# Kernel optimization log

Hardware: AMD Instinct MI355X
Metric: run time of the kernel (lower is better)

Reference implementation:

```python
import jax, jax.numpy as jnp
import numpy as np

S, WD, TD, CE, CH = 512, 300, 100, 20, 20   # seq len, word dim, tag dim, char emb dim, char lstm hidden
H = 512                                      # main LSTM hidden (per direction)
VOC, TVOC, CVOC, LAB, MAXW = 50000, 50, 100, 50, 16


def lstm_scan(x, W_ih, W_hh, b):
    """Unidirectional LSTM over x:[T,D] -> [T,hid]. PyTorch gate order i,f,g,o."""
    hid = W_hh.shape[1]
    def step(carry, xt):
        h, c = carry
        z = xt @ W_ih.T + h @ W_hh.T + b
        i, f, g, o = jnp.split(z, 4)
        c = jax.nn.sigmoid(f) * c + jax.nn.sigmoid(i) * jnp.tanh(g)
        h = jax.nn.sigmoid(o) * jnp.tanh(c)
        return (h, c), h
    h0 = jnp.zeros((hid,), x.dtype)
    _, hs = jax.lax.scan(step, (h0, h0), x)
    return hs


def setup_inputs() -> dict:
    key = jax.random.key(0)
    ks = jax.random.split(key, 40)
    n = lambda i, shape: jax.random.normal(ks[i], shape, jnp.float32) * 0.05
    return {
        "sentence": jax.random.randint(ks[0], (S,), 0, VOC),
        "tags": jax.random.randint(ks[1], (S,), 0, TVOC),
        "chars": jax.random.randint(ks[2], (S, MAXW), 0, CVOC),
        "char_lengths": jnp.maximum(1, jax.random.randint(ks[3], (S,), 0, MAXW + 1)),
        "best_arcs": jax.random.randint(ks[4], (S,), 0, S),
        "word_emb": n(5, (VOC, WD)),
        "tag_emb": n(6, (TVOC, TD)),
        "char_emb": n(7, (CVOC, CE)),
        "att_W": n(8, (1, CE)), "att_b": n(9, (1,)),
        "W_ih_f": n(10, (4 * H, WD + TD)), "W_hh_f": n(11, (4 * H, H)), "b_f": n(12, (4 * H,)),
        "W_ih_b": n(13, (4 * H, WD + TD)), "W_hh_b": n(14, (4 * H, H)), "b_b": n(15, (4 * H,)),
        "cW_ih": n(16, (4 * CH, CE)), "cW_hh": n(17, (4 * CH, CH)), "cb": n(18, (4 * CH,)),
        "arc_dep_W": n(19, (H, 2 * H)), "arc_dep_b": n(20, (H,)),
        "arc_head_W": n(21, (H, 2 * H)), "arc_head_b": n(22, (H,)),
        "label_dep_W": n(23, (H, 2 * H)), "label_dep_b": n(24, (H,)),
        "label_head_W": n(25, (H, 2 * H)), "label_head_b": n(26, (H,)),
        "biaff_arc_W": n(27, (H, H + 1)),
        "biaff_label_W": n(28, (LAB, H + 1, H + 1)),
    }


def reference(sentence, tags, chars, char_lengths, best_arcs,
              word_emb, tag_emb, char_emb, att_W, att_b,
              W_ih_f, W_hh_f, b_f, W_ih_b, W_hh_b, b_b,
              cW_ih, cW_hh, cb,
              arc_dep_W, arc_dep_b, arc_head_W, arc_head_b,
              label_dep_W, label_dep_b, label_head_W, label_head_b,
              biaff_arc_W, biaff_label_W):
    size = sentence.shape[0]
    we = word_emb[sentence]          # [S, WD]
    te = tag_emb[tags]               # [S, TD]

    # --- per-word char LSTM + attention (original python loop, here vmapped over padded words) ---
    ce = char_emb[chars]             # [S, Lmax, CE]
    def per_word(x, L):
        hs = lstm_scan(x, cW_ih, cW_hh, cb)                  # [Lmax, CH]
        hs = hs * (jnp.arange(x.shape[0]) < L)[:, None]      # zero padded steps
        gram = hs.T @ hs                                     # [CH, CH]
        return gram @ att_W.T + att_b                        # [CH, 1]
    char_feats = jax.vmap(per_word)(ce, char_lengths)        # [S, CH, 1]
    char_embeds = char_feats[:, :, 0].T                      # [CH, S] (cat dim=1 in torch)

    # --- main BiLSTM (dropout in eval mode = identity) ---
    embeds = jnp.concatenate([we, te], axis=1)               # [S, WD+TD]
    hf = lstm_scan(embeds, W_ih_f, W_hh_f, b_f)              # [S, H]
    hb = lstm_scan(embeds[::-1], W_ih_b, W_hh_b, b_b)[::-1]  # [S, H]
    lstm_out = jnp.concatenate([hf, hb], axis=1)             # [S, 2H]

    mlp = lambda W, b: jax.nn.relu(lstm_out @ W.T + b)       # MLP(2H -> H)
    arc_dep = mlp(arc_dep_W, arc_dep_b)
    arc_head = mlp(arc_head_W, arc_head_b)
    label_dep = mlp(label_dep_W, label_dep_b)
    label_head = mlp(label_head_W, label_head_b)

    ones = jnp.ones((size, 1), lstm_out.dtype)
    arc_head_a = jnp.concatenate([arc_head, ones], axis=1)     # [S, H+1]
    label_dep_a = jnp.concatenate([label_dep, ones], axis=1)   # [S, H+1]
    label_head_a = jnp.concatenate([label_head, ones], axis=1) # [S, H+1]

    arc_scores = jax.nn.softmax((arc_head_a @ biaff_arc_W.T) @ arc_dep.T, axis=1)  # [S, S]

    # label_head @ W_l @ label_dep^T for every label l -> [LAB, S, S]
    ls = jnp.einsum('sh,lhk,tk->lst', label_head_a, biaff_label_W, label_dep_a)
    sel = ls[:, best_arcs, jnp.arange(size)]                   # [LAB, S]
    label_scores = jax.nn.log_softmax(sel, axis=0)

    return (arc_scores, label_scores, char_embeds)
```

## Files before the change

kernel.cpp:

```cpp
#include <hip/hip_runtime.h>
#include <hip/hip_fp16.h>


static __device__ __forceinline__ float sigm(float x) { return 1.f / (1.f + __expf(-x)); }
static __device__ __forceinline__ float ftanh(float x) {
    x = fminf(15.f, fmaxf(-15.f, x));
    float e = __expf(2.f * x);
    return (e - 1.f) / (e + 1.f);
}

typedef _Float16 h2_t __attribute__((ext_vector_type(2)));
typedef _Float16 h8_t __attribute__((ext_vector_type(8)));
typedef float f4_t __attribute__((ext_vector_type(4)));
union U32H2 { unsigned u; h2_t h; unsigned short s[2]; };

static __device__ __forceinline__ float dot2f(unsigned wa, unsigned hb, float c) {
#if __has_builtin(__builtin_amdgcn_fdot2)
    U32H2 a, b; a.u = wa; b.u = hb;
    return __builtin_amdgcn_fdot2(a.h, b.h, c, false);
#else
    U32H2 a, b; a.u = wa; b.u = hb;
    return c + (float)a.h[0] * (float)b.h[0] + (float)a.h[1] * (float)b.h[1];
#endif
}
static __device__ __forceinline__ unsigned short f2h16(float x) {
    return __half_as_ushort(__float2half(x));
}

__global__ void gather_k(const int* __restrict__ sentence, const int* __restrict__ tags,
                         const float* __restrict__ word_emb, const float* __restrict__ tag_emb,
                         float* __restrict__ embeds) {
    int t = blockIdx.x;
    int w = sentence[t], tg = tags[t];
    for (int j = threadIdx.x; j < 400; j += blockDim.x) {
        float v = (j < 300) ? word_emb[w * 300 + j] : tag_emb[tg * 100 + (j - 300)];
        embeds[t * 400 + j] = v;
    }
}

static __device__ __forceinline__ void gemm_body_s(
    float* smemf, const float* __restrict__ A, int lda,
    const float* __restrict__ B, int ldb,
    const float* __restrict__ bias, int bias_stride,
    float* __restrict__ C, int ldc, int M, int K, int revA, int doRelu,
    int bm, int bn) {
    typedef float Row65[65];
    Row65* As = (Row65*)smemf;
    Row65* Bs = (Row65*)(smemf + 16 * 65);
    int tx = threadIdx.x & 15, ty = threadIdx.x >> 4;
    float acc[4][4] = {};
    for (int k0 = 0; k0 < K; k0 += 16) {
#pragma unroll
        for (int i = 0; i < 4; ++i) {
            int e = threadIdx.x + i * 256;
            int m = e >> 4, kk = e & 15;
            int row = bm + m; if (revA) row = M - 1 - row;
            As[kk][m] = A[(size_t)row * lda + k0 + kk];
            Bs[kk][m] = B[(size_t)(bn + m) * ldb + k0 + kk];
        }
        __syncthreads();
#pragma unroll
        for (int kk = 0; kk < 16; ++kk) {
            float a0 = As[kk][ty * 4 + 0], a1 = As[kk][ty * 4 + 1];
            float a2 = As[kk][ty * 4 + 2], a3 = As[kk][ty * 4 + 3];
            float b0 = Bs[kk][tx * 4 + 0], b1 = Bs[kk][tx * 4 + 1];
            float b2 = Bs[kk][tx * 4 + 2], b3 = Bs[kk][tx * 4 + 3];
            acc[0][0] += a0 * b0; acc[0][1] += a0 * b1; acc[0][2] += a0 * b2; acc[0][3] += a0 * b3;
            acc[1][0] += a1 * b0; acc[1][1] += a1 * b1; acc[1][2] += a1 * b2; acc[1][3] += a1 * b3;
            acc[2][0] += a2 * b0; acc[2][1] += a2 * b1; acc[2][2] += a2 * b2; acc[2][3] += a2 * b3;
            acc[3][0] += a3 * b0; acc[3][1] += a3 * b1; acc[3][2] += a3 * b2; acc[3][3] += a3 * b3;
        }
        __syncthreads();
    }
#pragma unroll
    for (int i = 0; i < 4; ++i) {
#pragma unroll
        for (int j = 0; j < 4; ++j) {
            int n = bn + tx * 4 + j;
            float v = acc[i][j];
            if (bias) v += bias[(size_t)n * bias_stride];
            if (doRelu) v = fmaxf(v, 0.f);
            C[(size_t)(bm + ty * 4 + i) * ldc + n] = v;
        }
    }
}

__global__ __launch_bounds__(256) void prep_k(
    const float* __restrict__ BW, _Float16* __restrict__ Bh,
    const int* __restrict__ chars, const int* __restrict__ char_lengths,
    const float* __restrict__ char_emb, const float* __restrict__ att_W,
    const float* __restrict__ att_b, const float* __restrict__ cW_ih,
    const float* __restrict__ cW_hh, const float* __restrict__ cb,
    float* __restrict__ out2,
    const float* __restrict__ embeds,
    const float* __restrict__ Wf, const float* __restrict__ bf, float* __restrict__ Cf,
    const float* __restrict__ Wb, const float* __restrict__ bb, float* __restrict__ Cb,
    const float* __restrict__ Warc, _Float16* __restrict__ W16arc) {
    __shared__ __align__(16) unsigned char smem[16384];
    int bid = blockIdx.x;
    int tid = threadIdx.x;

    if (bid < 4050) {
        typedef _Float16 TsRow[68];
        TsRow* Ts = (TsRow*)smem;
        int lb = bid / 81, rem = bid % 81;
        int h0 = (rem % 9) * 64, k0 = (rem / 9) * 64;
        const float* Bl = BW + (size_t)lb * 513 * 513;
        _Float16* BhL = Bh + (size_t)lb * 576 * 544;
        int tr = tid >> 4, tc = tid & 15;
#pragma unroll
        for (int i = 0; i < 4; ++i) {
            int hl = tr + i * 16;
            int h = h0 + hl;
#pragma unroll
            for (int j = 0; j < 4; ++j) {
                int k = k0 + tc * 4 + j;
                float v = (h < 513 && k < 513) ? Bl[(size_t)h * 513 + k] : 0.f;
                Ts[hl][tc * 4 + j] = (_Float16)v;
            }
        }
        __syncthreads();
        int cr = tid >> 2, hb = (tid & 3) * 16;
        int hg = h0 + hb;
        if (hg < 544) {
            __align__(16) _Float16 tmp[16];
#pragma unroll
            for (int j = 0; j < 16; ++j) tmp[j] = Ts[hb + j][cr];
            uint4* dst = (uint4*)(BhL + (size_t)(k0 + cr) * 544 + hg);
            dst[0] = ((const uint4*)tmp)[0];
            dst[1] = ((const uint4*)tmp)[1];
        }
    } else if (bid < 4050 + 512) {
        float* Wih = (float*)smem;
        float* Whh2 = Wih + 1600;
        float* cbs = Whh2 + 1600;
        float* attsh = cbs + 80;
        float* xsh = attsh + 20;
        float* hsh = xsh + 20;
        float* prodsh = hsh + 20;
        int wd = bid - 4050;
        for (int i = tid; i < 1600; i += 256) { Wih[i] = cW_ih[i]; Whh2[i] = cW_hh[i]; }
        for (int i = tid; i < 80; i += 256) cbs[i] = cb[i];
        if (tid < 20) { attsh[tid] = att_W[tid]; hsh[tid] = 0.f; }
        __syncthreads();

        int L = char_lengths[wd];
        float c = 0.f, accj = 0.f;
        for (int t = 0; t < 16; ++t) {
            if (tid < 20) xsh[tid] = char_emb[(size_t)chars[wd * 16 + t] * 20 + tid];
            __syncthreads();
            float hn = 0.f;
            if (tid < 20) {
                float z[4];
#pragma unroll
                for (int q = 0; q < 4; ++q) {
                    int rr = q * 20 + tid;
                    float sacc = cbs[rr];
                    for (int d = 0; d < 20; ++d)
                        sacc += Wih[rr * 20 + d] * xsh[d] + Whh2[rr * 20 + d] * hsh[d];
                    z[q] = sacc;
                }
                c = sigm(z[1]) * c + sigm(z[0]) * ftanh(z[2]);
                hn = sigm(z[3]) * ftanh(c);
            }
            __syncthreads();
            if (tid < 20) { hsh[tid] = hn; prodsh[tid] = hn * attsh[tid]; }
            __syncthreads();
            if (tid < 20 && t < L) {
                float st = 0.f;
                for (int k = 0; k < 20; ++k) st += prodsh[k];
                accj += hn * st;
            }
            __syncthreads();
        }
        if (tid < 20) out2[tid * 512 + wd] = accj + att_b[0];
    } else if (bid < 4050 + 512 + 512) {
        int idx = bid - (4050 + 512);
        int z = idx >> 8, rem = idx & 255;
        int bn = (rem & 31) * 64;
        int bm = (rem >> 5) * 64;
        const float* W = z ? Wb : Wf;
        const float* bias = z ? bb : bf;
        float* C = z ? Cb : Cf;
        gemm_body_s((float*)smem, embeds, 400, W, 400, bias, 1, C, 2048,
                    512, 400, z, 0, bm, bn);
    } else {
        int t = bid - (4050 + 512 + 512);
        for (int j = tid; j < 544; j += 256)
            W16arc[(size_t)t * 544 + j] = (_Float16)((j < 513) ? Warc[(size_t)t * 513 + j] : 0.f);
    }
}

__global__ void hconv_k(const float* __restrict__ hw0, const float* __restrict__ hw1,
                        const float* __restrict__ hw2, const float* __restrict__ hw3,
                        _Float16* __restrict__ Wh16) {
    size_t e0 = ((size_t)blockIdx.x * 256 + threadIdx.x) * 8;
    int mat = (int)(e0 >> 19);
    size_t off = e0 & 524287;
    const float* src = (mat == 0 ? hw0 : mat == 1 ? hw1 : mat == 2 ? hw2 : hw3) + off;
    float4 f0 = ((const float4*)src)[0];
    float4 f1 = ((const float4*)src)[1];
    __align__(16) _Float16 hv[8];
    hv[0] = (_Float16)f0.x; hv[1] = (_Float16)f0.y;
    hv[2] = (_Float16)f0.z; hv[3] = (_Float16)f0.w;
    hv[4] = (_Float16)f1.x; hv[5] = (_Float16)f1.y;
    hv[6] = (_Float16)f1.z; hv[7] = (_Float16)f1.w;
    *(uint4*)(Wh16 + e0) = *(const uint4*)hv;
}

__global__ __launch_bounds__(256) void lstm_k(
    const float* __restrict__ W_hh_f, const float* __restrict__ W_hh_b,
    const float* __restrict__ xpf, const float* __restrict__ xpb,
    _Float16* __restrict__ lstmh, unsigned long long* hq) {
    int wg = blockIdx.x;
    int dir = wg >> 4, s = wg & 15;
    int tid = threadIdx.x;
    int wv = tid >> 6;
    int lane = tid & 63;
    int g = tid & 31, p = tid >> 5;
    const float* Whh = dir ? W_hh_b : W_hh_f;
    const float* xp = dir ? xpb : xpf;

    __shared__ float red[2][1024];

    unsigned Wreg[4][32];
#pragma unroll
    for (int q = 0; q < 4; ++q) {
        int gr = q * 512 + s * 32 + g;
        const float* wrow = Whh + (size_t)gr * 512 + p * 64;
#pragma unroll
        for (int u = 0; u < 32; ++u) {
            unsigned lo = f2h16(wrow[2 * u]);
            unsigned hi = f2h16(wrow[2 * u + 1]);
            Wreg[q][u] = lo | (hi << 16);
        }
    }

    float c = 0.f;
    unsigned long long* hbase = hq + dir * 512;
    int qidx = wv * 64 + lane;

    for (int t = 0; t < 512; ++t) {
        float x0 = 0.f, x1 = 0.f, x2 = 0.f, x3 = 0.f;
        if (tid < 32) {
            const float* x = xp + (size_t)t * 2048;
            int col = s * 32 + tid;
            x0 = x[col]; x1 = x[512 + col]; x2 = x[1024 + col]; x3 = x[1536 + col];
        }

        unsigned long long* hin = hbase + (t & 1) * 256;
        unsigned tag = (unsigned)t & 0xffffu;
        unsigned long long v = __hip_atomic_load(hin + qidx, __ATOMIC_RELAXED,
                                                 __HIP_MEMORY_SCOPE_AGENT);
        while ((((unsigned)(v >> 16)) & 0xffffu) != tag || ((unsigned)(v >> 48)) != tag)
            v = __hip_atomic_load(hin + qidx, __ATOMIC_RELAXED, __HIP_MEMORY_SCOPE_AGENT);
        unsigned hw = (unsigned)(v & 0xffffu) | (((unsigned)((v >> 32) & 0xffffu)) << 16);

        float a0 = 0.f, a1 = 0.f, a2 = 0.f, a3 = 0.f;
        int half_base = lane & 32;
#pragma unroll
        for (int u = 0; u < 32; ++u) {
            unsigned hwu = (unsigned)__shfl((int)hw, half_base + u);
            a0 = dot2f(Wreg[0][u], hwu, a0);
            a1 = dot2f(Wreg[1][u], hwu, a1);
            a2 = dot2f(Wreg[2][u], hwu, a2);
            a3 = dot2f(Wreg[3][u], hwu, a3);
        }
        float* r = &red[t & 1][p * 128 + g * 4];
        r[0] = a0; r[1] = a1; r[2] = a2; r[3] = a3;
        __syncthreads();

        if (tid < 32) {
            float z0 = 0.f, z1 = 0.f, z2 = 0.f, z3 = 0.f;
            const float* rb = red[t & 1];
#pragma unroll
            for (int pp = 0; pp < 8; ++pp) {
                const float* rr = rb + pp * 128 + tid * 4;
                z0 += rr[0]; z1 += rr[1]; z2 += rr[2]; z3 += rr[3];
            }
            z0 += x0; z1 += x1; z2 += x2; z3 += x3;
            c = sigm(z1) * c + sigm(z0) * ftanh(z2);
            float hn = sigm(z3) * ftanh(c);
            int col = s * 32 + tid;
            int row = dir ? (511 - t) : t;
            lstmh[(size_t)row * 1024 + dir * 512 + col] = (_Float16)hn;

            unsigned tw = (unsigned)f2h16(hn) | (((unsigned)(t + 1) & 0xffffu) << 16);
            unsigned other = (unsigned)__shfl_down((int)tw, 1);
            if ((tid & 1) == 0) {
                unsigned long long qv = (unsigned long long)tw |
                                        ((unsigned long long)other << 32);
                __hip_atomic_store(hbase + ((t + 1) & 1) * 256 + (col >> 1), qv,
                                   __ATOMIC_RELAXED, __HIP_MEMORY_SCOPE_AGENT);
            }
        }
    }
}

__global__ __launch_bounds__(256) void heads_mfma(
    const _Float16* __restrict__ A, const _Float16* __restrict__ Wh,
    const float* __restrict__ b0, const float* __restrict__ b1,
    const float* __restrict__ b2, const float* __restrict__ b3,
    _Float16* __restrict__ AD16, _Float16* __restrict__ AH16,
    float* __restrict__ LD, _Float16* __restrict__ LH16) {
    __shared__ _Float16 As[64][40];
    __shared__ _Float16 Bs[64][40];
    int hd = blockIdx.z;
    int m0 = blockIdx.y * 64, n0 = blockIdx.x * 64;
    const _Float16* Bp = Wh + (size_t)hd * 512 * 1024;
    const float* bias = (hd == 0) ? b0 : (hd == 1) ? b1 : (hd == 2) ? b2 : b3;
    int tid = threadIdx.x;
    int w = tid >> 6, lane = tid & 63, m = lane & 15, q = lane >> 4;
    int srow = tid >> 2, scol = (tid & 3) * 8;

    f4_t acc[4];
#pragma unroll
    for (int cc = 0; cc < 4; ++cc) acc[cc] = 0;

    for (int k0 = 0; k0 < 1024; k0 += 32) {
        uint4 ad = *(const uint4*)(A + (size_t)(m0 + srow) * 1024 + k0 + scol);
        uint4 bd = *(const uint4*)(Bp + (size_t)(n0 + srow) * 1024 + k0 + scol);
        __syncthreads();
        *(uint4*)(&As[srow][scol]) = ad;
        *(uint4*)(&Bs[srow][scol]) = bd;
        __syncthreads();
        h8_t a  = *(const h8_t*)(&As[w * 16 + m][q * 8]);
        h8_t bb0 = *(const h8_t*)(&Bs[ 0 + m][q * 8]);
        h8_t bb1 = *(const h8_t*)(&Bs[16 + m][q * 8]);
        h8_t bb2 = *(const h8_t*)(&Bs[32 + m][q * 8]);
        h8_t bb3 = *(const h8_t*)(&Bs[48 + m][q * 8]);
        acc[0] = __builtin_amdgcn_mfma_f32_16x16x32_f16(a, bb0, acc[0], 0, 0, 0);
        acc[1] = __builtin_amdgcn_mfma_f32_16x16x32_f16(a, bb1, acc[1], 0, 0, 0);
        acc[2] = __builtin_amdgcn_mfma_f32_16x16x32_f16(a, bb2, acc[2], 0, 0, 0);
        acc[3] = __builtin_amdgcn_mfma_f32_16x16x32_f16(a, bb3, acc[3], 0, 0, 0);
    }
#pragma unroll
    for (int r = 0; r < 4; ++r) {
        int row = m0 + w * 16 + q * 4 + r;
#pragma unroll
        for (int cc = 0; cc < 4; ++cc) {
            int ncol = n0 + cc * 16 + m;
            float v = fmaxf(acc[cc][r] + bias[ncol], 0.f);
            if (hd == 2)      LD[(size_t)row * 512 + ncol] = v;
            else if (hd == 0) AD16[(size_t)row * 512 + ncol] = (_Float16)v;
            else {
                _Float16* dst = (hd == 1) ? AH16 : LH16;
                dst[(size_t)row * 544 + ncol] = (_Float16)v;
            }
        }
    }
    if ((hd == 1 || hd == 3) && blockIdx.x == 7 && tid < 64) {
        _Float16* dst = (hd == 1) ? AH16 : LH16;
        int row = m0 + tid;
        dst[(size_t)row * 544 + 512] = (_Float16)1.f;
        for (int j = 513; j < 544; ++j) dst[(size_t)row * 544 + j] = (_Float16)0.f;
    }
}

__global__ void uv2_k(const int* __restrict__ best_arcs,
                      const _Float16* __restrict__ LH16, const float* __restrict__ LD,
                      _Float16* __restrict__ Uh, float* __restrict__ V) {
    int t = blockIdx.x;
    int ba = best_arcs[t];
    const unsigned* src = (const unsigned*)(LH16 + (size_t)ba * 544);
    unsigned* dst = (unsigned*)(Uh + (size_t)t * 544);
    for (int j = threadIdx.x; j < 272; j += blockDim.x) dst[j] = src[j];
    for (int j = threadIdx.x; j < 516; j += blockDim.x)
        V[t * 516 + j] = (j < 512) ? LD[(size_t)t * 512 + j] : (j == 512 ? 1.f : 0.f);
}

__global__ __launch_bounds__(256) void gemm16_mfma(
    const _Float16* __restrict__ A, int lda,
    const _Float16* __restrict__ B, int ldb, int K,
    _Float16* __restrict__ C16, float* __restrict__ C32) {
    __shared__ _Float16 As[64][40];
    __shared__ _Float16 Bs[64][40];
    int m0 = blockIdx.y * 64, n0 = blockIdx.x * 64;
    int tid = threadIdx.x;
    int w = tid >> 6, lane = tid & 63, m = lane & 15, q = lane >> 4;
    int srow = tid >> 2, scol = (tid & 3) * 8;

    f4_t acc[4];
#pragma unroll
    for (int cc = 0; cc < 4; ++cc) acc[cc] = 0;

    for (int k0 = 0; k0 < K; k0 += 32) {
        uint4 ad = *(const uint4*)(A + (size_t)(m0 + srow) * lda + k0 + scol);
        uint4 bd = *(const uint4*)(B + (size_t)(n0 + srow) * ldb + k0 + scol);
        __syncthreads();
        *(uint4*)(&As[srow][scol]) = ad;
        *(uint4*)(&Bs[srow][scol]) = bd;
        __syncthreads();
        h8_t a  = *(const h8_t*)(&As[w * 16 + m][q * 8]);
        h8_t b0 = *(const h8_t*)(&Bs[ 0 + m][q * 8]);
        h8_t b1 = *(const h8_t*)(&Bs[16 + m][q * 8]);
        h8_t b2 = *(const h8_t*)(&Bs[32 + m][q * 8]);
        h8_t b3 = *(const h8_t*)(&Bs[48 + m][q * 8]);
        acc[0] = __builtin_amdgcn_mfma_f32_16x16x32_f16(a, b0, acc[0], 0, 0, 0);
        acc[1] = __builtin_amdgcn_mfma_f32_16x16x32_f16(a, b1, acc[1], 0, 0, 0);
        acc[2] = __builtin_amdgcn_mfma_f32_16x16x32_f16(a, b2, acc[2], 0, 0, 0);
        acc[3] = __builtin_amdgcn_mfma_f32_16x16x32_f16(a, b3, acc[3], 0, 0, 0);
    }
#pragma unroll
    for (int r = 0; r < 4; ++r) {
        int row = m0 + w * 16 + q * 4 + r;
#pragma unroll
        for (int cc = 0; cc < 4; ++cc) {
            int ncol = n0 + cc * 16 + m;
            if (C16) C16[(size_t)row * 512 + ncol] = (_Float16)acc[cc][r];
            else     C32[(size_t)row * 512 + ncol] = acc[cc][r];
        }
    }
}

__global__ __launch_bounds__(256) void label_mfma(
    const _Float16* __restrict__ Uh, const _Float16* __restrict__ Bh,
    const float* __restrict__ V, float* __restrict__ sel) {
    __shared__ _Float16 Us[64][40];
    __shared__ _Float16 Bs[64][40];
    int l = blockIdx.z;
    int t0 = blockIdx.y * 64, k0 = blockIdx.x * 64;
    int tid = threadIdx.x;
    int w = tid >> 6, lane = tid & 63, m = lane & 15, q = lane >> 4;
    const _Float16* Bl = Bh + (size_t)l * 576 * 544;
    int srow = tid >> 2, scol = (tid & 3) * 8;

    f4_t acc[4];
#pragma unroll
    for (int c = 0; c < 4; ++c) acc[c] = 0;

    for (int h0 = 0; h0 < 544; h0 += 32) {
        uint4 ud = *(const uint4*)(Uh + (size_t)(t0 + srow) * 544 + h0 + scol);
        uint4 bd = *(const uint4*)(Bl + (size_t)(k0 + srow) * 544 + h0 + scol);
        __syncthreads();
        *(uint4*)(&Us[srow][scol]) = ud;
        *(uint4*)(&Bs[srow][scol]) = bd;
        __syncthreads();
        h8_t a  = *(const h8_t*)(&Us[w * 16 + m][q * 8]);
        h8_t b0 = *(const h8_t*)(&Bs[ 0 + m][q * 8]);
        h8_t b1 = *(const h8_t*)(&Bs[16 + m][q * 8]);
        h8_t b2 = *(const h8_t*)(&Bs[32 + m][q * 8]);
        h8_t b3 = *(const h8_t*)(&Bs[48 + m][q * 8]);
        acc[0] = __builtin_amdgcn_mfma_f32_16x16x32_f16(a, b0, acc[0], 0, 0, 0);
        acc[1] = __builtin_amdgcn_mfma_f32_16x16x32_f16(a, b1, acc[1], 0, 0, 0);
        acc[2] = __builtin_amdgcn_mfma_f32_16x16x32_f16(a, b2, acc[2], 0, 0, 0);
        acc[3] = __builtin_amdgcn_mfma_f32_16x16x32_f16(a, b3, acc[3], 0, 0, 0);
    }

    float* selp = sel + (size_t)l * 512;
#pragma unroll
    for (int r = 0; r < 4; ++r) {
        int t = t0 + w * 16 + q * 4 + r;
        float vsum = 0.f;
#pragma unroll
        for (int c = 0; c < 4; ++c) {
            int k = k0 + c * 16 + m;
            float vv = (k < 513) ? V[(size_t)t * 516 + k] : 0.f;
            vsum += acc[c][r] * vv;
        }
#pragma unroll
        for (int off = 1; off < 16; off <<= 1)
            vsum += __shfl_xor(vsum, off);
        if (m == 0) atomicAdd(selp + t, vsum);
    }
}

__global__ __launch_bounds__(256) void softmax_rows(float* __restrict__ Smat) {
    __shared__ float sdata[256];
    int i = blockIdx.x, tid = threadIdx.x;
    float* row = Smat + (size_t)i * 512;
    float m = -1e30f;
    for (int j = tid; j < 512; j += 256) m = fmaxf(m, row[j]);
    sdata[tid] = m; __syncthreads();
    for (int off = 128; off > 0; off >>= 1) {
        if (tid < off) sdata[tid] = fmaxf(sdata[tid], sdata[tid + off]);
        __syncthreads();
    }
    m = sdata[0]; __syncthreads();
    float ssum = 0.f;
    for (int j = tid; j < 512; j += 256) { float e = __expf(row[j] - m); row[j] = e; ssum += e; }
    sdata[tid] = ssum; __syncthreads();
    for (int off = 128; off > 0; off >>= 1) {
        if (tid < off) sdata[tid] += sdata[tid + off];
        __syncthreads();
    }
    float inv = 1.f / sdata[0];
    for (int j = tid; j < 512; j += 256) row[j] *= inv;
}

__global__ void lsm_k(const float* __restrict__ sel, float* __restrict__ out1) {
    int t = blockIdx.x * blockDim.x + threadIdx.x;
    if (t >= 512) return;
    float m = -1e30f;
    for (int l = 0; l < 50; ++l) m = fmaxf(m, sel[l * 512 + t]);
    float ssum = 0.f;
    for (int l = 0; l < 50; ++l) ssum += __expf(sel[l * 512 + t] - m);
    float lse = m + __logf(ssum);
    for (int l = 0; l < 50; ++l) out1[l * 512 + t] = sel[l * 512 + t] - lse;
}

extern "C" void kernel_launch(void* const* d_in, const int* in_sizes, int n_in,
                              void* d_out, int out_size, void* d_ws, size_t ws_size,
                              hipStream_t stream) {
    const int* sentence     = (const int*)d_in[0];
    const int* tags         = (const int*)d_in[1];
    const int* chars        = (const int*)d_in[2];
    const int* char_lengths = (const int*)d_in[3];
    const int* best_arcs    = (const int*)d_in[4];
    const float* word_emb   = (const float*)d_in[5];
    const float* tag_emb    = (const float*)d_in[6];
    const float* char_emb   = (const float*)d_in[7];
    const float* att_W      = (const float*)d_in[8];
    const float* att_b      = (const float*)d_in[9];
    const float* W_ih_f     = (const float*)d_in[10];
    const float* W_hh_f     = (const float*)d_in[11];
    const float* b_f        = (const float*)d_in[12];
    const float* W_ih_b     = (const float*)d_in[13];
    const float* W_hh_b     = (const float*)d_in[14];
    const float* b_b        = (const float*)d_in[15];
    const float* cW_ih      = (const float*)d_in[16];
    const float* cW_hh      = (const float*)d_in[17];
    const float* cb         = (const float*)d_in[18];
    const float* arc_dep_W  = (const float*)d_in[19];
    const float* arc_dep_b  = (const float*)d_in[20];
    const float* arc_head_W = (const float*)d_in[21];
    const float* arc_head_b = (const float*)d_in[22];
    const float* label_dep_W  = (const float*)d_in[23];
    const float* label_dep_b  = (const float*)d_in[24];
    const float* label_head_W = (const float*)d_in[25];
    const float* label_head_b = (const float*)d_in[26];
    const float* biaff_arc_W   = (const float*)d_in[27];
    const float* biaff_label_W = (const float*)d_in[28];

    float* ws = (float*)d_ws;
    float* out = (float*)d_out;

    const size_t o_embeds = 0;
    const size_t o_Wh16   = 0;
    const size_t o_V      = 204800;
    const size_t o_Uh     = 468992;
    const size_t o_xf     = 1134592;
    const size_t o_xb     = 2183168;
    const size_t o_lstmh  = 3231744;
    const size_t o_heads  = 3493888;
    const size_t o_LD     = o_heads + 0;
    const size_t o_AD16   = o_heads + 262144;
    const size_t o_AH16   = o_heads + 393216;
    const size_t o_LH16   = o_heads + 532480;
    const size_t o_P16    = o_heads + 671744;
    const size_t o_Warc16 = o_heads + 802816;
    const size_t o_sel    = 4542464;
    const size_t o_hG     = 4568064;
    const size_t o_Bh     = 4570112;

    hipMemsetAsync(ws + o_hG, 0, 8192, stream);
    hipMemsetAsync(ws + o_sel, 0, 25600 * sizeof(float), stream);

    gather_k<<<512, 128, 0, stream>>>(sentence, tags, word_emb, tag_emb, ws + o_embeds);

    prep_k<<<5586, 256, 0, stream>>>(
        biaff_label_W, (_Float16*)(ws + o_Bh),
        chars, char_lengths, char_emb, att_W, att_b, cW_ih, cW_hh, cb,
        out + 287744,
        ws + o_embeds,
        W_ih_f, b_f, ws + o_xf,
        W_ih_b, b_b, ws + o_xb,
        biaff_arc_W, (_Float16*)(ws + o_Warc16));

    hconv_k<<<1024, 256, 0, stream>>>(arc_dep_W, arc_head_W, label_dep_W, label_head_W,
                                      (_Float16*)(ws + o_Wh16));

    lstm_k<<<32, 256, 0, stream>>>(W_hh_f, W_hh_b, ws + o_xf, ws + o_xb,
                                   (_Float16*)(ws + o_lstmh),
                                   (unsigned long long*)(ws + o_hG));

    heads_mfma<<<dim3(8, 8, 4), 256, 0, stream>>>(
        (const _Float16*)(ws + o_lstmh), (const _Float16*)(ws + o_Wh16),
        arc_dep_b, arc_head_b, label_dep_b, label_head_b,
        (_Float16*)(ws + o_AD16), (_Float16*)(ws + o_AH16),
        ws + o_LD, (_Float16*)(ws + o_LH16));

    uv2_k<<<512, 128, 0, stream>>>(best_arcs, (const _Float16*)(ws + o_LH16),
                                   ws + o_LD, (_Float16*)(ws + o_Uh), ws + o_V);

    gemm16_mfma<<<dim3(8, 8), 256, 0, stream>>>(
        (const _Float16*)(ws + o_AH16), 544, (const _Float16*)(ws + o_Warc16), 544, 544,
        (_Float16*)(ws + o_P16), nullptr);
    gemm16_mfma<<<dim3(8, 8), 256, 0, stream>>>(
        (const _Float16*)(ws + o_P16), 512, (const _Float16*)(ws + o_AD16), 512, 512,
        nullptr, out);
    softmax_rows<<<512, 256, 0, stream>>>(out);

    label_mfma<<<dim3(9, 8, 50), 256, 0, stream>>>(
        (const _Float16*)(ws + o_Uh), (const _Float16*)(ws + o_Bh),
        ws + o_V, ws + o_sel);
    lsm_k<<<2, 256, 0, stream>>>(ws + o_sel, out + 262144);
}
```

Measured before the change: 1.363 ms.

## Overlap LSTM recurrence with weight preprocessing in one fused launch

```diff
diff --git a/kernel.cpp b/kernel.cpp
--- a/kernel.cpp
+++ b/kernel.cpp
@@ -27,36 +27,122 @@
     return __half_as_ushort(__float2half(x));
 }
 
-__global__ void gather_k(const int* __restrict__ sentence, const int* __restrict__ tags,
-                         const float* __restrict__ word_emb, const float* __restrict__ tag_emb,
-                         float* __restrict__ embeds) {
-    int t = blockIdx.x;
-    int w = sentence[t], tg = tags[t];
-    for (int j = threadIdx.x; j < 400; j += blockDim.x) {
-        float v = (j < 300) ? word_emb[w * 300 + j] : tag_emb[tg * 100 + (j - 300)];
-        embeds[t * 400 + j] = v;
-    }
-}
-
-static __device__ __forceinline__ void gemm_body_s(
-    float* smemf, const float* __restrict__ A, int lda,
-    const float* __restrict__ B, int ldb,
-    const float* __restrict__ bias, int bias_stride,
-    float* __restrict__ C, int ldc, int M, int K, int revA, int doRelu,
-    int bm, int bn) {
+static __device__ __forceinline__ unsigned long long hq_ld(const unsigned long long* p) {
+    return __hip_atomic_load(p, __ATOMIC_RELAXED, __HIP_MEMORY_SCOPE_AGENT);
+}
+static __device__ __forceinline__ void hq_st(unsigned long long* p, unsigned long long v) {
+    __hip_atomic_store(p, v, __ATOMIC_RELAXED, __HIP_MEMORY_SCOPE_AGENT);
+}
+
+static __device__ void lstm_core(int dir, int s, int tid,
+                                 const float* __restrict__ Whh,
+                                 const float* __restrict__ xp,
+                                 _Float16* __restrict__ lstmh,
+                                 unsigned long long* __restrict__ hq,
+                                 float* __restrict__ red ) {
+    int lane = tid & 63;
+    int g = tid & 31, p = tid >> 5;
+
+    unsigned Wreg[4][32];
+#pragma unroll
+    for (int q = 0; q < 4; ++q) {
+        int gr = q * 512 + s * 32 + g;
+        const float* wrow = Whh + (size_t)gr * 512 + p * 64;
+#pragma unroll
+        for (int u = 0; u < 32; ++u) {
+            unsigned lo = f2h16(wrow[2 * u]);
+            unsigned hi = f2h16(wrow[2 * u + 1]);
+            Wreg[q][u] = lo | (hi << 16);
+        }
+    }
+
+    float c = 0.f;
+    unsigned long long* hbase = hq + dir * 512;
+    int qidx = tid;
+
+    for (int t = 0; t < 512; ++t) {
+        float x0 = 0.f, x1 = 0.f, x2 = 0.f, x3 = 0.f;
+        if (tid < 32) {
+            const float* x = xp + (size_t)t * 2048;
+            int col = s * 32 + tid;
+            x0 = x[col]; x1 = x[512 + col]; x2 = x[1024 + col]; x3 = x[1536 + col];
+        }
+
+        unsigned long long* hin = hbase + (t & 1) * 256;
+        unsigned tag = (unsigned)t & 0xffffu;
+        unsigned long long v = hq_ld(hin + qidx);
+        while ((((unsigned)(v >> 16)) & 0xffffu) != tag || ((unsigned)(v >> 48)) != tag)
+            v = hq_ld(hin + qidx);
+        unsigned hw = (unsigned)(v & 0xffffu) | (((unsigned)((v >> 32) & 0xffffu)) << 16);
+
+        float a0 = 0.f, a1 = 0.f, a2 = 0.f, a3 = 0.f;
+        int half_base = lane & 32;
+#pragma unroll
+        for (int u = 0; u < 32; ++u) {
+            unsigned hwu = (unsigned)__shfl((int)hw, half_base + u);
+            a0 = dot2f(Wreg[0][u], hwu, a0);
+            a1 = dot2f(Wreg[1][u], hwu, a1);
+            a2 = dot2f(Wreg[2][u], hwu, a2);
+            a3 = dot2f(Wreg[3][u], hwu, a3);
+        }
+        float* r = red + (t & 1) * 1024 + p * 128 + g * 4;
+        r[0] = a0; r[1] = a1; r[2] = a2; r[3] = a3;
+        __syncthreads();
+
+        if (tid < 32) {
+            float z0 = 0.f, z1 = 0.f, z2 = 0.f, z3 = 0.f;
+            const float* rb = red + (t & 1) * 1024;
+#pragma unroll
+            for (int pp = 0; pp < 8; ++pp) {
+                const float* rr = rb + pp * 128 + tid * 4;
+                z0 += rr[0]; z1 += rr[1]; z2 += rr[2]; z3 += rr[3];
+            }
+            z0 += x0; z1 += x1; z2 += x2; z3 += x3;
+            c = sigm(z1) * c + sigm(z0) * ftanh(z2);
+            float hn = sigm(z3) * ftanh(c);
+            int col = s * 32 + tid;
+            int row = dir ? (511 - t) : t;
+            lstmh[(size_t)row * 1024 + dir * 512 + col] = (_Float16)hn;
+
+            unsigned tw = (unsigned)f2h16(hn) | (((unsigned)(t + 1) & 0xffffu) << 16);
+            unsigned other = (unsigned)__shfl_down((int)tw, 1);
+            if ((tid & 1) == 0) {
+                unsigned long long qv = (unsigned long long)tw |
+                                        ((unsigned long long)other << 32);
+                hq_st(hbase + ((t + 1) & 1) * 256 + (col >> 1), qv);
+            }
+        }
+    }
+}
+
+__global__ __launch_bounds__(256) void xproj_k(
+    const int* __restrict__ sentence, const int* __restrict__ tags,
+    const float* __restrict__ word_emb, const float* __restrict__ tag_emb,
+    const float* __restrict__ Wf, const float* __restrict__ bf, float* __restrict__ Cf,
+    const float* __restrict__ Wb, const float* __restrict__ bb, float* __restrict__ Cb) {
+    __shared__ float smemf[2 * 16 * 65];
     typedef float Row65[65];
     Row65* As = (Row65*)smemf;
     Row65* Bs = (Row65*)(smemf + 16 * 65);
+    int idx = blockIdx.x;
+    int z = idx >> 8, rem = idx & 255;
+    int bn = (rem & 31) * 64, bm = (rem >> 5) * 64;
+    const float* W = z ? Wb : Wf;
+    const float* bias = z ? bb : bf;
+    float* C = z ? Cb : Cf;
     int tx = threadIdx.x & 15, ty = threadIdx.x >> 4;
     float acc[4][4] = {};
-    for (int k0 = 0; k0 < K; k0 += 16) {
+    for (int k0 = 0; k0 < 400; k0 += 16) {
 #pragma unroll
         for (int i = 0; i < 4; ++i) {
             int e = threadIdx.x + i * 256;
             int m = e >> 4, kk = e & 15;
-            int row = bm + m; if (revA) row = M - 1 - row;
-            As[kk][m] = A[(size_t)row * lda + k0 + kk];
-            Bs[kk][m] = B[(size_t)(bn + m) * ldb + k0 + kk];
+            int row = bm + m; if (z) row = 511 - row;
+            int k = k0 + kk;
+            float av = (k < 300) ? word_emb[(size_t)sentence[row] * 300 + k]
+                                 : tag_emb[(size_t)tags[row] * 100 + (k - 300)];
+            As[kk][m] = av;
+            Bs[kk][m] = W[(size_t)(bn + m) * 400 + k];
         }
         __syncthreads();
 #pragma unroll
@@ -77,60 +163,35 @@
 #pragma unroll
         for (int j = 0; j < 4; ++j) {
             int n = bn + tx * 4 + j;
-            float v = acc[i][j];
-            if (bias) v += bias[(size_t)n * bias_stride];
-            if (doRelu) v = fmaxf(v, 0.f);
-            C[(size_t)(bm + ty * 4 + i) * ldc + n] = v;
-        }
-    }
-}
-
-__global__ __launch_bounds__(256) void prep_k(
+            C[(size_t)(bm + ty * 4 + i) * 2048 + n] = acc[i][j] + bias[n];
+        }
+    }
+}
+
+__global__ __launch_bounds__(256) void fused_k(
+    const float* __restrict__ W_hh_f, const float* __restrict__ W_hh_b,
+    const float* __restrict__ xpf, const float* __restrict__ xpb,
+    _Float16* __restrict__ lstmh, unsigned long long* __restrict__ hq,
     const float* __restrict__ BW, _Float16* __restrict__ Bh,
     const int* __restrict__ chars, const int* __restrict__ char_lengths,
     const float* __restrict__ char_emb, const float* __restrict__ att_W,
     const float* __restrict__ att_b, const float* __restrict__ cW_ih,
     const float* __restrict__ cW_hh, const float* __restrict__ cb,
     float* __restrict__ out2,
-    const float* __restrict__ embeds,
-    const float* __restrict__ Wf, const float* __restrict__ bf, float* __restrict__ Cf,
-    const float* __restrict__ Wb, const float* __restrict__ bb, float* __restrict__ Cb,
-    const float* __restrict__ Warc, _Float16* __restrict__ W16arc) {
+    const float* __restrict__ Warc, _Float16* __restrict__ W16arc,
+    const float* __restrict__ hw0, const float* __restrict__ hw1,
+    const float* __restrict__ hw2, const float* __restrict__ hw3,
+    _Float16* __restrict__ Wh16) {
     __shared__ __align__(16) unsigned char smem[16384];
     int bid = blockIdx.x;
     int tid = threadIdx.x;
 
-    if (bid < 4050) {
-        typedef _Float16 TsRow[68];
-        TsRow* Ts = (TsRow*)smem;
-        int lb = bid / 81, rem = bid % 81;
-        int h0 = (rem % 9) * 64, k0 = (rem / 9) * 64;
-        const float* Bl = BW + (size_t)lb * 513 * 513;
-        _Float16* BhL = Bh + (size_t)lb * 576 * 544;
-        int tr = tid >> 4, tc = tid & 15;
-#pragma unroll
-        for (int i = 0; i < 4; ++i) {
-            int hl = tr + i * 16;
-            int h = h0 + hl;
-#pragma unroll
-            for (int j = 0; j < 4; ++j) {
-                int k = k0 + tc * 4 + j;
-                float v = (h < 513 && k < 513) ? Bl[(size_t)h * 513 + k] : 0.f;
-                Ts[hl][tc * 4 + j] = (_Float16)v;
-            }
-        }
-        __syncthreads();
-        int cr = tid >> 2, hb = (tid & 3) * 16;
-        int hg = h0 + hb;
-        if (hg < 544) {
-            __align__(16) _Float16 tmp[16];
-#pragma unroll
-            for (int j = 0; j < 16; ++j) tmp[j] = Ts[hb + j][cr];
-            uint4* dst = (uint4*)(BhL + (size_t)(k0 + cr) * 544 + hg);
-            dst[0] = ((const uint4*)tmp)[0];
-            dst[1] = ((const uint4*)tmp)[1];
-        }
-    } else if (bid < 4050 + 512) {
+    if (bid < 32) {
+        int dir = bid >> 4, s = bid & 15;
+        const float* Whh = dir ? W_hh_b : W_hh_f;
+        const float* xp = dir ? xpb : xpf;
+        lstm_core(dir, s, tid, Whh, xp, lstmh, hq, (float*)smem);
+    } else if (bid < 544) {
         float* Wih = (float*)smem;
         float* Whh2 = Wih + 1600;
         float* cbs = Whh2 + 1600;
@@ -138,7 +199,7 @@
         float* xsh = attsh + 20;
         float* hsh = xsh + 20;
         float* prodsh = hsh + 20;
-        int wd = bid - 4050;
+        int wd = bid - 32;
         for (int i = tid; i < 1600; i += 256) { Wih[i] = cW_ih[i]; Whh2[i] = cW_hh[i]; }
         for (int i = tid; i < 80; i += 256) cbs[i] = cb[i];
         if (tid < 20) { attsh[tid] = att_W[tid]; hsh[tid] = 0.f; }
@@ -174,125 +235,53 @@
             __syncthreads();
         }
         if (tid < 20) out2[tid * 512 + wd] = accj + att_b[0];
-    } else if (bid < 4050 + 512 + 512) {
-        int idx = bid - (4050 + 512);
-        int z = idx >> 8, rem = idx & 255;
-        int bn = (rem & 31) * 64;
-        int bm = (rem >> 5) * 64;
-        const float* W = z ? Wb : Wf;
-        const float* bias = z ? bb : bf;
-        float* C = z ? Cb : Cf;
-        gemm_body_s((float*)smem, embeds, 400, W, 400, bias, 1, C, 2048,
-                    512, 400, z, 0, bm, bn);
-    } else {
-        int t = bid - (4050 + 512 + 512);
+    } else if (bid < 1568) {
+        size_t e0 = ((size_t)(bid - 544) * 256 + tid) * 8;
+        int mat = (int)(e0 >> 19);
+        size_t off = e0 & 524287;
+        const float* src = (mat == 0 ? hw0 : mat == 1 ? hw1 : mat == 2 ? hw2 : hw3) + off;
+        float4 f0 = ((const float4*)src)[0];
+        float4 f1 = ((const float4*)src)[1];
+        __align__(16) _Float16 hv[8];
+        hv[0] = (_Float16)f0.x; hv[1] = (_Float16)f0.y;
+        hv[2] = (_Float16)f0.z; hv[3] = (_Float16)f0.w;
+        hv[4] = (_Float16)f1.x; hv[5] = (_Float16)f1.y;
+        hv[6] = (_Float16)f1.z; hv[7] = (_Float16)f1.w;
+        *(uint4*)(Wh16 + e0) = *(const uint4*)hv;
+    } else if (bid < 2080) {
+        int t = bid - 1568;
         for (int j = tid; j < 544; j += 256)
             W16arc[(size_t)t * 544 + j] = (_Float16)((j < 513) ? Warc[(size_t)t * 513 + j] : 0.f);
-    }
-}
-
-__global__ void hconv_k(const float* __restrict__ hw0, const float* __restrict__ hw1,
-                        const float* __restrict__ hw2, const float* __restrict__ hw3,
-                        _Float16* __restrict__ Wh16) {
-    size_t e0 = ((size_t)blockIdx.x * 256 + threadIdx.x) * 8;
-    int mat = (int)(e0 >> 19);
-    size_t off = e0 & 524287;
-    const float* src = (mat == 0 ? hw0 : mat == 1 ? hw1 : mat == 2 ? hw2 : hw3) + off;
-    float4 f0 = ((const float4*)src)[0];
-    float4 f1 = ((const float4*)src)[1];
-    __align__(16) _Float16 hv[8];
-    hv[0] = (_Float16)f0.x; hv[1] = (_Float16)f0.y;
-    hv[2] = (_Float16)f0.z; hv[3] = (_Float16)f0.w;
-    hv[4] = (_Float16)f1.x; hv[5] = (_Float16)f1.y;
-    hv[6] = (_Float16)f1.z; hv[7] = (_Float16)f1.w;
-    *(uint4*)(Wh16 + e0) = *(const uint4*)hv;
-}
-
-__global__ __launch_bounds__(256) void lstm_k(
-    const float* __restrict__ W_hh_f, const float* __restrict__ W_hh_b,
-    const float* __restrict__ xpf, const float* __restrict__ xpb,
-    _Float16* __restrict__ lstmh, unsigned long long* hq) {
-    int wg = blockIdx.x;
-    int dir = wg >> 4, s = wg & 15;
-    int tid = threadIdx.x;
-    int wv = tid >> 6;
-    int lane = tid & 63;
-    int g = tid & 31, p = tid >> 5;
-    const float* Whh = dir ? W_hh_b : W_hh_f;
-    const float* xp = dir ? xpb : xpf;
-
-    __shared__ float red[2][1024];
-
-    unsigned Wreg[4][32];
-#pragma unroll
-    for (int q = 0; q < 4; ++q) {
-        int gr = q * 512 + s * 32 + g;
-        const float* wrow = Whh + (size_t)gr * 512 + p * 64;
-#pragma unroll
-        for (int u = 0; u < 32; ++u) {
-            unsigned lo = f2h16(wrow[2 * u]);
-            unsigned hi = f2h16(wrow[2 * u + 1]);
-            Wreg[q][u] = lo | (hi << 16);
-        }
-    }
-
-    float c = 0.f;
-    unsigned long long* hbase = hq + dir * 512;
-    int qidx = wv * 64 + lane;
-
-    for (int t = 0; t < 512; ++t) {
-        float x0 = 0.f, x1 = 0.f, x2 = 0.f, x3 = 0.f;
-        if (tid < 32) {
-            const float* x = xp + (size_t)t * 2048;
-            int col = s * 32 + tid;
-            x0 = x[col]; x1 = x[512 + col]; x2 = x[1024 + col]; x3 = x[1536 + col];
-        }
-
-        unsigned long long* hin = hbase + (t & 1) * 256;
-        unsigned tag = (unsigned)t & 0xffffu;
-        unsigned long long v = __hip_atomic_load(hin + qidx, __ATOMIC_RELAXED,
-                                                 __HIP_MEMORY_SCOPE_AGENT);
-        while ((((unsigned)(v >> 16)) & 0xffffu) != tag || ((unsigned)(v >> 48)) != tag)
-            v = __hip_atomic_load(hin + qidx, __ATOMIC_RELAXED, __HIP_MEMORY_SCOPE_AGENT);
-        unsigned hw = (unsigned)(v & 0xffffu) | (((unsigned)((v >> 32) & 0xffffu)) << 16);
-
-        float a0 = 0.f, a1 = 0.f, a2 = 0.f, a3 = 0.f;
-        int half_base = lane & 32;
-#pragma unroll
-        for (int u = 0; u < 32; ++u) {
-            unsigned hwu = (unsigned)__shfl((int)hw, half_base + u);
-            a0 = dot2f(Wreg[0][u], hwu, a0);
-            a1 = dot2f(Wreg[1][u], hwu, a1);
-            a2 = dot2f(Wreg[2][u], hwu, a2);
-            a3 = dot2f(Wreg[3][u], hwu, a3);
-        }
-        float* r = &red[t & 1][p * 128 + g * 4];
-        r[0] = a0; r[1] = a1; r[2] = a2; r[3] = a3;
-        __syncthreads();
-
-        if (tid < 32) {
-            float z0 = 0.f, z1 = 0.f, z2 = 0.f, z3 = 0.f;
-            const float* rb = red[t & 1];
-#pragma unroll
-            for (int pp = 0; pp < 8; ++pp) {
-                const float* rr = rb + pp * 128 + tid * 4;
-                z0 += rr[0]; z1 += rr[1]; z2 += rr[2]; z3 += rr[3];
+    } else {
+        typedef _Float16 TsRow[68];
+        TsRow* Ts = (TsRow*)smem;
+        int b2 = bid - 2080;
+        int lb = b2 / 81, rem = b2 % 81;
+        int h0 = (rem % 9) * 64, k0 = (rem / 9) * 64;
+        const float* Bl = BW + (size_t)lb * 513 * 513;
+        _Float16* BhL = Bh + (size_t)lb * 576 * 544;
+        int tr = tid >> 4, tc = tid & 15;
+#pragma unroll
+        for (int i = 0; i < 4; ++i) {
+            int hl = tr + i * 16;
+            int h = h0 + hl;
+#pragma unroll
+            for (int j = 0; j < 4; ++j) {
+                int k = k0 + tc * 4 + j;
+                float v = (h < 513 && k < 513) ? Bl[(size_t)h * 513 + k] : 0.f;
+                Ts[hl][tc * 4 + j] = (_Float16)v;
             }
-            z0 += x0; z1 += x1; z2 += x2; z3 += x3;
-            c = sigm(z1) * c + sigm(z0) * ftanh(z2);
-            float hn = sigm(z3) * ftanh(c);
-            int col = s * 32 + tid;
-            int row = dir ? (511 - t) : t;
-            lstmh[(size_t)row * 1024 + dir * 512 + col] = (_Float16)hn;
-
-            unsigned tw = (unsigned)f2h16(hn) | (((unsigned)(t + 1) & 0xffffu) << 16);
-            unsigned other = (unsigned)__shfl_down((int)tw, 1);
-            if ((tid & 1) == 0) {
-                unsigned long long qv = (unsigned long long)tw |
-                                        ((unsigned long long)other << 32);
-                __hip_atomic_store(hbase + ((t + 1) & 1) * 256 + (col >> 1), qv,
-                                   __ATOMIC_RELAXED, __HIP_MEMORY_SCOPE_AGENT);
-            }
+        }
+        __syncthreads();
+        int cr = tid >> 2, hb = (tid & 3) * 16;
+        int hg = h0 + hb;
+        if (hg < 544) {
+            __align__(16) _Float16 tmp[16];
+#pragma unroll
+            for (int j = 0; j < 16; ++j) tmp[j] = Ts[hb + j][cr];
+            uint4* dst = (uint4*)(BhL + (size_t)(k0 + cr) * 544 + hg);
+            dst[0] = ((const uint4*)tmp)[0];
+            dst[1] = ((const uint4*)tmp)[1];
         }
     }
 }
@@ -535,7 +524,6 @@
     float* ws = (float*)d_ws;
     float* out = (float*)d_out;
 
-    const size_t o_embeds = 0;
     const size_t o_Wh16   = 0;
     const size_t o_V      = 204800;
     const size_t o_Uh     = 468992;
@@ -556,23 +544,19 @@
     hipMemsetAsync(ws + o_hG, 0, 8192, stream);
     hipMemsetAsync(ws + o_sel, 0, 25600 * sizeof(float), stream);
 
-    gather_k<<<512, 128, 0, stream>>>(sentence, tags, word_emb, tag_emb, ws + o_embeds);
-
-    prep_k<<<5586, 256, 0, stream>>>(
+    xproj_k<<<512, 256, 0, stream>>>(sentence, tags, word_emb, tag_emb,
+                                     W_ih_f, b_f, ws + o_xf,
+                                     W_ih_b, b_b, ws + o_xb);
+
+    fused_k<<<6130, 256, 0, stream>>>(
+        W_hh_f, W_hh_b, ws + o_xf, ws + o_xb,
+        (_Float16*)(ws + o_lstmh), (unsigned long long*)(ws + o_hG),
         biaff_label_W, (_Float16*)(ws + o_Bh),
         chars, char_lengths, char_emb, att_W, att_b, cW_ih, cW_hh, cb,
         out + 287744,
-        ws + o_embeds,
-        W_ih_f, b_f, ws + o_xf,
-        W_ih_b, b_b, ws + o_xb,
-        biaff_arc_W, (_Float16*)(ws + o_Warc16));
-
-    hconv_k<<<1024, 256, 0, stream>>>(arc_dep_W, arc_head_W, label_dep_W, label_head_W,
-                                      (_Float16*)(ws + o_Wh16));
-
-    lstm_k<<<32, 256, 0, stream>>>(W_hh_f, W_hh_b, ws + o_xf, ws + o_xb,
-                                   (_Float16*)(ws + o_lstmh),
-                                   (unsigned long long*)(ws + o_hG));
+        biaff_arc_W, (_Float16*)(ws + o_Warc16),
+        arc_dep_W, arc_head_W, label_dep_W, label_head_W,
+        (_Float16*)(ws + o_Wh16));
 
     heads_mfma<<<dim3(8, 8, 4), 256, 0, stream>>>(
         (const _Float16*)(ws + o_lstmh), (const _Float16*)(ws + o_Wh16),
```

New measurement: 1.293 ms. -5.2%, faster.
